# Kernel optimization log

Hardware: AMD Instinct MI355X
Metric: run time of the kernel (lower is better)

Reference implementation:

```python
import jax, jax.numpy as jnp
import numpy as np

B, T, N, D = 32, 50, 100, 4
E = N * (N - 1)
N_IN, N_HID, N_OUT = T * D, 256, 4


def _mlp(x, w1, b1, w2, b2):
    # Linear -> ReLU -> (dropout=0) -> Linear
    return jax.nn.relu(x @ w1 + b1) @ w2 + b2


def setup_inputs() -> dict:
    key = jax.random.key(0)
    ks = jax.random.split(key, 12)
    # fully-connected directed graph, no self loops
    idx = np.array([(i, j) for i in range(N) for j in range(N) if i != j], dtype=np.int64)
    recv, sendr = idx[:, 0], idx[:, 1]
    rec = jnp.asarray(np.eye(N, dtype=np.float32)[recv])    # [E, N]
    send = jnp.asarray(np.eye(N, dtype=np.float32)[sendr])  # [E, N]

    def lin(k, fan_in, fan_out):
        kw, kb = jax.random.split(k)
        w = jax.random.normal(kw, (fan_in, fan_out), jnp.float32) * 0.02
        b = jax.random.normal(kb, (fan_out,), jnp.float32) * 0.02
        return w, b

    x = jax.random.normal(ks[0], (B, T, N, D), jnp.float32)
    w1a, b1a = lin(ks[1], N_IN, N_HID)
    w1b, b1b = lin(ks[2], N_HID, N_HID)
    w2a, b2a = lin(ks[3], 2 * N_HID, N_HID)
    w2b, b2b = lin(ks[4], N_HID, N_HID)
    w3a, b3a = lin(ks[5], N_HID, N_HID)
    w3b, b3b = lin(ks[6], N_HID, N_HID)
    w4a, b4a = lin(ks[7], 3 * N_HID, N_HID)
    w4b, b4b = lin(ks[8], N_HID, N_HID)
    wo, bo = lin(ks[9], N_HID, N_OUT)
    return {"x": x, "rec": rec, "send": send,
            "w1a": w1a, "b1a": b1a, "w1b": w1b, "b1b": b1b,
            "w2a": w2a, "b2a": b2a, "w2b": w2b, "b2b": b2b,
            "w3a": w3a, "b3a": b3a, "w3b": w3b, "b3b": b3b,
            "w4a": w4a, "b4a": b4a, "w4b": w4b, "b4b": b4b,
            "wo": wo, "bo": bo}


def reference(x, rec, send,
              w1a, b1a, w1b, b1b,
              w2a, b2a, w2b, b2b,
              w3a, b3a, w3b, b3b,
              w4a, b4a, w4b, b4b,
              wo, bo):
    # [B, T, N, D] -> [B, N, T*D]
    h = jnp.transpose(x, (0, 2, 1, 3)).reshape(x.shape[0], x.shape[2], -1)
    h = _mlp(h, w1a, b1a, w1b, b1b)                       # [B, N, H]
    # v2e: gather receiver/sender node states to edges
    e = jnp.concatenate([jnp.einsum('en,bnh->beh', rec, h),
                         jnp.einsum('en,bnh->beh', send, h)], axis=2)  # [B, E, 2H]
    e = _mlp(e, w2a, b2a, w2b, b2b)                       # [B, E, H]
    x_skip = e
    # e2v: scatter edges back to nodes, normalize by n_nodes
    v = jnp.einsum('en,beh->bnh', rec, e) / e.shape[-2] * (e.shape[-2] / rec.shape[1])
    v = jnp.einsum('en,beh->bnh', rec, e) / rec.shape[1]  # incoming / incoming.size(1)=N
    v = _mlp(v, w3a, b3a, w3b, b3b)                       # [B, N, H]
    e2 = jnp.concatenate([jnp.einsum('en,bnh->beh', rec, v),
                          jnp.einsum('en,bnh->beh', send, v)], axis=2)  # [B, E, 2H]
    e2 = jnp.concatenate([e2, x_skip], axis=2)            # [B, E, 3H]
    e2 = _mlp(e2, w4a, b4a, w4b, b4b)                     # [B, E, H]
    return e2 @ wo + bo                                   # [B, E, n_out]
```

## Files before the change

kernel.cpp:

```cpp
#include <hip/hip_runtime.h>
#include <hip/hip_bf16.h>
#include <stdint.h>


typedef __attribute__((ext_vector_type(8))) short short8;
typedef __attribute__((ext_vector_type(4))) float float4v;
typedef __attribute__((ext_vector_type(4))) unsigned short ushort4v;

__device__ inline float bf2f(unsigned short u) {
    union { unsigned int i; float f; } v; v.i = ((unsigned int)u) << 16; return v.f;
}

#if __has_builtin(__builtin_amdgcn_cvt_pk_bf16_f32)
typedef __attribute__((ext_vector_type(2))) __bf16 bf16x2;
__device__ inline unsigned int f2bf_pk(float a, float b) {
    union { bf16x2 v; unsigned int u; } c;
    c.v = __builtin_amdgcn_cvt_pk_bf16_f32(a, b);
    return c.u;
}
__device__ inline unsigned short f2bf(float f) {
    return (unsigned short)(f2bf_pk(f, f) & 0xFFFFu);
}
#else
__device__ inline unsigned short f2bf(float f) {
    union { float f; unsigned int i; } v; v.f = f;
    unsigned int i = v.i;
    return (unsigned short)((i + 0x7FFFu + ((i >> 16) & 1u)) >> 16);
}
__device__ inline unsigned int f2bf_pk(float a, float b) {
    return (unsigned int)f2bf(a) | ((unsigned int)f2bf(b) << 16);
}
#endif

__global__ __launch_bounds__(256) void prep_kernel(
        const float* __restrict__ x,
        const float* __restrict__ w1a, const float* __restrict__ w1b,
        const float* __restrict__ w2a, const float* __restrict__ w2b,
        const float* __restrict__ w3a, const float* __restrict__ w3b,
        const float* __restrict__ w4a, const float* __restrict__ b4a,
        const float* __restrict__ w4b, const float* __restrict__ b4b,
        const float* __restrict__ wo,  const float* __restrict__ bo,
        const float* __restrict__ b2b,
        unsigned short* __restrict__ Wp1a, unsigned short* __restrict__ Wp1b,
        unsigned short* __restrict__ Wp2r, unsigned short* __restrict__ Wp2s,
        unsigned short* __restrict__ Wp2b, unsigned short* __restrict__ Wp3a,
        unsigned short* __restrict__ Wp3b, unsigned short* __restrict__ Wp4r,
        unsigned short* __restrict__ Wp4s, unsigned short* __restrict__ Wpz,
        unsigned short* __restrict__ Wfp, float* __restrict__ bfv,
        float* __restrict__ b4ap, float* __restrict__ b2bs,
        unsigned short* __restrict__ hin) {
    int bx = blockIdx.x;
    int tid = threadIdx.x;
    if (bx < 2272) {
        const float* W; unsigned short* Wp; int Kin; int b0;
        if      (bx <  224) { W = w1a;             Wp = Wp1a; Kin = 200; b0 = 0;    }
        else if (bx <  480) { W = w1b;             Wp = Wp1b; Kin = 256; b0 = 224;  }
        else if (bx <  736) { W = w2a;             Wp = Wp2r; Kin = 256; b0 = 480;  }
        else if (bx <  992) { W = w2a + 256 * 256; Wp = Wp2s; Kin = 256; b0 = 736;  }
        else if (bx < 1248) { W = w2b;             Wp = Wp2b; Kin = 256; b0 = 992;  }
        else if (bx < 1504) { W = w3a;             Wp = Wp3a; Kin = 256; b0 = 1248; }
        else if (bx < 1760) { W = w3b;             Wp = Wp3b; Kin = 256; b0 = 1504; }
        else if (bx < 2016) { W = w4a;             Wp = Wp4r; Kin = 256; b0 = 1760; }
        else                { W = w4a + 256 * 256; Wp = Wp4s; Kin = 256; b0 = 2016; }
        int idx = (bx - b0) * 256 + tid;
        int k = idx >> 8, n = idx & 255;
        unsigned short v = (k < Kin) ? f2bf(W[k * 256 + n]) : (unsigned short)0;
        Wp[((size_t)(k >> 5) * 256 + n) * 32 + (k & 31)] = v;
    } else if (bx < 2528) {
        int k = bx - 2272, c = tid;
        float s = 0.f;
        for (int t = 0; t < 256; ++t)
            s += w2b[k * 256 + t] * w4a[(size_t)(512 + t) * 256 + c];
        Wpz[((size_t)(k >> 5) * 256 + c) * 32 + (k & 31)] = f2bf(s);
    } else if (bx < 2530) {
        int k = tid;
        if (bx == 2528) {
            float a[4] = {0.f, 0.f, 0.f, 0.f};
            for (int c = 0; c < 256; ++c) {
                float wv = w4b[k * 256 + c];
                #pragma unroll
                for (int o = 0; o < 4; ++o) a[o] += wv * wo[c * 4 + o];
            }
            #pragma unroll
            for (int n = 0; n < 16; ++n)
                Wfp[(size_t)(k >> 5) * 512 + n * 32 + (k & 31)] =
                    (n < 4) ? f2bf(a[n]) : (unsigned short)0;
            if (k < 4) {
                float s = bo[k];
                for (int c = 0; c < 256; ++c) s += b4b[c] * wo[c * 4 + k];
                bfv[k] = s;
            }
        } else {
            float s = b4a[k];
            for (int t = 0; t < 256; ++t)
                s += b2b[t] * w4a[(size_t)(512 + t) * 256 + k];
            b4ap[k] = s;
            b2bs[k] = 0.99f * b2b[k];
        }
    } else {
        int idx = (bx - 2530) * 256 + tid;
        if (idx < 3200 * 224) {
            int row = idx / 224;
            int c = idx - row * 224;
            int b = row / 100, n = row - b * 100;
            unsigned short v = 0;
            if (c < 200) {
                int t = c >> 2, d = c & 3;
                v = f2bf(x[(((size_t)(b * 50 + t)) * 100 + n) * 4 + d]);
            }
            hin[(size_t)row * 224 + c] = v;
        }
    }
}

__global__ __launch_bounds__(512) void node_fusedA_kernel(
        const unsigned short* __restrict__ hin,
        const unsigned short* __restrict__ Wp1a, const float* __restrict__ b1a,
        const unsigned short* __restrict__ Wp1b, const float* __restrict__ b1b,
        const unsigned short* __restrict__ Wp2r, const float* __restrict__ b2a,
        const unsigned short* __restrict__ Wp2s,
        unsigned short* __restrict__ U, unsigned short* __restrict__ Hs) {
    __shared__ __align__(16) unsigned short t1s[16 * 264];
    __shared__ __align__(16) unsigned short hs2[16 * 264];
    const int m0 = blockIdx.x * 16;
    const int tid  = threadIdx.x;
    const int wave = tid >> 6;
    const int lane = tid & 63;
    const int l15  = lane & 15;
    const int quad = lane >> 4;
    const int n0   = wave * 32;
    const int koff = quad * 8;

    {
        float4v acc[2];
        acc[0] = (float4v)(0.0f); acc[1] = (float4v)(0.0f);
        for (int kb = 0; kb < 7; ++kb) {
            short8 af = *(const short8*)(hin + (size_t)(m0 + l15) * 224 + kb * 32 + koff);
            #pragma unroll
            for (int ni = 0; ni < 2; ++ni) {
                short8 bf = *(const short8*)(Wp1a + ((size_t)kb * 256 + n0 + ni * 16 + l15) * 32 + koff);
                acc[ni] = __builtin_amdgcn_mfma_f32_16x16x32_bf16(af, bf, acc[ni], 0, 0, 0);
            }
        }
        #pragma unroll
        for (int ni = 0; ni < 2; ++ni) {
            int col = n0 + ni * 16 + l15;
            float bv = b1a[col];
            #pragma unroll
            for (int r = 0; r < 4; ++r) {
                float v = acc[ni][r] + bv;
                v = v > 0.f ? v : 0.f;
                t1s[(quad * 4 + r) * 264 + col] = f2bf(v);
            }
        }
    }
    __syncthreads();

    {
        float4v acc[2];
        acc[0] = (float4v)(0.0f); acc[1] = (float4v)(0.0f);
        for (int kb = 0; kb < 8; ++kb) {
            short8 af = *(const short8*)(&t1s[l15 * 264 + kb * 32 + koff]);
            #pragma unroll
            for (int ni = 0; ni < 2; ++ni) {
                short8 bf = *(const short8*)(Wp1b + ((size_t)kb * 256 + n0 + ni * 16 + l15) * 32 + koff);
                acc[ni] = __builtin_amdgcn_mfma_f32_16x16x32_bf16(af, bf, acc[ni], 0, 0, 0);
            }
        }
        #pragma unroll
        for (int ni = 0; ni < 2; ++ni) {
            int col = n0 + ni * 16 + l15;
            float bv = b1b[col];
            #pragma unroll
            for (int r = 0; r < 4; ++r)
                hs2[(quad * 4 + r) * 264 + col] = f2bf(acc[ni][r] + bv);
        }
    }
    __syncthreads();

    {
        float4v aU[2], aH[2];
        aU[0] = (float4v)(0.0f); aU[1] = (float4v)(0.0f);
        aH[0] = (float4v)(0.0f); aH[1] = (float4v)(0.0f);
        for (int kb = 0; kb < 8; ++kb) {
            short8 af = *(const short8*)(&hs2[l15 * 264 + kb * 32 + koff]);
            #pragma unroll
            for (int ni = 0; ni < 2; ++ni) {
                short8 bu = *(const short8*)(Wp2r + ((size_t)kb * 256 + n0 + ni * 16 + l15) * 32 + koff);
                short8 bh = *(const short8*)(Wp2s + ((size_t)kb * 256 + n0 + ni * 16 + l15) * 32 + koff);
                aU[ni] = __builtin_amdgcn_mfma_f32_16x16x32_bf16(af, bu, aU[ni], 0, 0, 0);
                aH[ni] = __builtin_amdgcn_mfma_f32_16x16x32_bf16(af, bh, aH[ni], 0, 0, 0);
            }
        }
        #pragma unroll
        for (int ni = 0; ni < 2; ++ni) {
            int col = n0 + ni * 16 + l15;
            float bv = b2a[col];
            #pragma unroll
            for (int r = 0; r < 4; ++r) {
                size_t o = (size_t)(m0 + quad * 4 + r) * 256 + col;
                U[o]  = f2bf(aU[ni][r] + bv);
                Hs[o] = f2bf(aH[ni][r]);
            }
        }
    }
}

__global__ __launch_bounds__(512) void node_fusedC_kernel(
        const unsigned short* __restrict__ Ssc,
        const unsigned short* __restrict__ Wp2b, const float* __restrict__ b2bs,
        const unsigned short* __restrict__ Wp3a, const float* __restrict__ b3a,
        const unsigned short* __restrict__ Wp3b, const float* __restrict__ b3b,
        const unsigned short* __restrict__ Wp4r, const float* __restrict__ b4ap,
        const unsigned short* __restrict__ Wp4s,
        unsigned short* __restrict__ C4, unsigned short* __restrict__ Vs) {
    __shared__ __align__(16) unsigned short buf0[16 * 264];
    __shared__ __align__(16) unsigned short buf1[16 * 264];
    const int m0 = blockIdx.x * 16;
    const int tid  = threadIdx.x;
    const int wave = tid >> 6;
    const int lane = tid & 63;
    const int l15  = lane & 15;
    const int quad = lane >> 4;
    const int n0   = wave * 32;
    const int koff = quad * 8;

    {
        float4v acc[2];
        acc[0] = (float4v)(0.0f); acc[1] = (float4v)(0.0f);
        for (int kb = 0; kb < 8; ++kb) {
            short8 af = *(const short8*)(Ssc + (size_t)(m0 + l15) * 256 + kb * 32 + koff);
            #pragma unroll
            for (int ni = 0; ni < 2; ++ni) {
                short8 bf = *(const short8*)(Wp2b + ((size_t)kb * 256 + n0 + ni * 16 + l15) * 32 + koff);
                acc[ni] = __builtin_amdgcn_mfma_f32_16x16x32_bf16(af, bf, acc[ni], 0, 0, 0);
            }
        }
        #pragma unroll
        for (int ni = 0; ni < 2; ++ni) {
            int col = n0 + ni * 16 + l15;
            float bv = b2bs[col];
            #pragma unroll
            for (int r = 0; r < 4; ++r)
                buf0[(quad * 4 + r) * 264 + col] = f2bf(acc[ni][r] + bv);
        }
    }
    __syncthreads();

    {
        float4v acc[2];
        acc[0] = (float4v)(0.0f); acc[1] = (float4v)(0.0f);
        for (int kb = 0; kb < 8; ++kb) {
            short8 af = *(const short8*)(&buf0[l15 * 264 + kb * 32 + koff]);
            #pragma unroll
            for (int ni = 0; ni < 2; ++ni) {
                short8 bf = *(const short8*)(Wp3a + ((size_t)kb * 256 + n0 + ni * 16 + l15) * 32 + koff);
                acc[ni] = __builtin_amdgcn_mfma_f32_16x16x32_bf16(af, bf, acc[ni], 0, 0, 0);
            }
        }
        #pragma unroll
        for (int ni = 0; ni < 2; ++ni) {
            int col = n0 + ni * 16 + l15;
            float bv = b3a[col];
            #pragma unroll
            for (int r = 0; r < 4; ++r) {
                float v = acc[ni][r] + bv;
                v = v > 0.f ? v : 0.f;
                buf1[(quad * 4 + r) * 264 + col] = f2bf(v);
            }
        }
    }
    __syncthreads();

    {
        float4v acc[2];
        acc[0] = (float4v)(0.0f); acc[1] = (float4v)(0.0f);
        for (int kb = 0; kb < 8; ++kb) {
            short8 af = *(const short8*)(&buf1[l15 * 264 + kb * 32 + koff]);
            #pragma unroll
            for (int ni = 0; ni < 2; ++ni) {
                short8 bf = *(const short8*)(Wp3b + ((size_t)kb * 256 + n0 + ni * 16 + l15) * 32 + koff);
                acc[ni] = __builtin_amdgcn_mfma_f32_16x16x32_bf16(af, bf, acc[ni], 0, 0, 0);
            }
        }
        __syncthreads();
        #pragma unroll
        for (int ni = 0; ni < 2; ++ni) {
            int col = n0 + ni * 16 + l15;
            float bv = b3b[col];
            #pragma unroll
            for (int r = 0; r < 4; ++r)
                buf0[(quad * 4 + r) * 264 + col] = f2bf(acc[ni][r] + bv);
        }
    }
    __syncthreads();

    {
        float4v aC[2], aV[2];
        aC[0] = (float4v)(0.0f); aC[1] = (float4v)(0.0f);
        aV[0] = (float4v)(0.0f); aV[1] = (float4v)(0.0f);
        for (int kb = 0; kb < 8; ++kb) {
            short8 af = *(const short8*)(&buf0[l15 * 264 + kb * 32 + koff]);
            #pragma unroll
            for (int ni = 0; ni < 2; ++ni) {
                short8 bc = *(const short8*)(Wp4r + ((size_t)kb * 256 + n0 + ni * 16 + l15) * 32 + koff);
                short8 bv = *(const short8*)(Wp4s + ((size_t)kb * 256 + n0 + ni * 16 + l15) * 32 + koff);
                aC[ni] = __builtin_amdgcn_mfma_f32_16x16x32_bf16(af, bc, aC[ni], 0, 0, 0);
                aV[ni] = __builtin_amdgcn_mfma_f32_16x16x32_bf16(af, bv, aV[ni], 0, 0, 0);
            }
        }
        #pragma unroll
        for (int ni = 0; ni < 2; ++ni) {
            int col = n0 + ni * 16 + l15;
            float bv = b4ap[col];
            #pragma unroll
            for (int r = 0; r < 4; ++r) {
                size_t o = (size_t)(m0 + quad * 4 + r) * 256 + col;
                C4[o] = f2bf(aC[ni][r] + bv);
                Vs[o] = f2bf(aV[ni][r]);
            }
        }
    }
}

__global__ __launch_bounds__(256) void colsum_kernel(
        const unsigned short* __restrict__ U, const unsigned short* __restrict__ Hs,
        unsigned short* __restrict__ Ssc) {
    const int g = blockIdx.x * 4 + (threadIdx.x >> 6);
    const int b = g / 100, i = g - b * 100;
    const int c = (threadIdx.x & 63) * 4;
    ushort4v uv = *(const ushort4v*)(U + (size_t)g * 256 + c);
    const float u0 = bf2f(uv[0]), u1 = bf2f(uv[1]), u2 = bf2f(uv[2]), u3 = bf2f(uv[3]);
    const unsigned short* base = Hs + (size_t)b * 100 * 256 + c;
    float s0 = 0.f, s1 = 0.f, s2 = 0.f, s3 = 0.f;
    #pragma unroll 4
    for (int j = 0; j < 100; ++j) {
        ushort4v hv = *(const ushort4v*)(base + (size_t)j * 256);
        float v0 = u0 + bf2f(hv[0]); s0 += (v0 > 0.f ? v0 : 0.f);
        float v1 = u1 + bf2f(hv[1]); s1 += (v1 > 0.f ? v1 : 0.f);
        float v2 = u2 + bf2f(hv[2]); s2 += (v2 > 0.f ? v2 : 0.f);
        float v3 = u3 + bf2f(hv[3]); s3 += (v3 > 0.f ? v3 : 0.f);
    }
    {
        ushort4v hv = *(const ushort4v*)(base + (size_t)i * 256);
        float v0 = u0 + bf2f(hv[0]); s0 -= (v0 > 0.f ? v0 : 0.f);
        float v1 = u1 + bf2f(hv[1]); s1 -= (v1 > 0.f ? v1 : 0.f);
        float v2 = u2 + bf2f(hv[2]); s2 -= (v2 > 0.f ? v2 : 0.f);
        float v3 = u3 + bf2f(hv[3]); s3 -= (v3 > 0.f ? v3 : 0.f);
    }
    unsigned int* dst = (unsigned int*)(Ssc + (size_t)g * 256 + c);
    dst[0] = f2bf_pk(s0 * 0.01f, s1 * 0.01f);
    dst[1] = f2bf_pk(s2 * 0.01f, s3 * 0.01f);
}

__global__ __launch_bounds__(512, 6) void edge_phaseB_kernel(
        const unsigned short* __restrict__ Hs, const unsigned short* __restrict__ Vs,
        const unsigned short* __restrict__ U, const unsigned short* __restrict__ C4,
        const unsigned short* __restrict__ Wpz, const unsigned short* __restrict__ Wfp,
        const float* __restrict__ bfv,
        float* __restrict__ out) {
    __shared__ __align__(16) unsigned short t2s[64 * 264];
    const int g = blockIdx.x, hb = blockIdx.y;
    const int b = g / 100, nr = g - b * 100;
    const int nrows = hb ? 49 : 50;
    const int k0 = hb * 50;
    const int tid  = threadIdx.x;
    const int wave = tid >> 6;
    const int lane = tid & 63;
    const int l15  = lane & 15;
    const int quad = lane >> 4;
    const int n0   = wave * 32;
    const int koff = quad * 8;

    {
        const int c = lane * 4;
        ushort4v uv = *(const ushort4v*)(U + (size_t)g * 256 + c);
        float u0 = bf2f(uv[0]), u1 = bf2f(uv[1]), u2 = bf2f(uv[2]), u3 = bf2f(uv[3]);
        for (int r = wave; r < 64; r += 8) {
            unsigned int p01 = 0, p23 = 0;
            if (r < nrows) {
                int k = k0 + r;
                int j = k + (k >= nr ? 1 : 0);
                ushort4v hv = *(const ushort4v*)(Hs + (size_t)(b * 100 + j) * 256 + c);
                float t0 = u0 + bf2f(hv[0]); t0 = t0 > 0.f ? t0 : 0.f;
                float t1 = u1 + bf2f(hv[1]); t1 = t1 > 0.f ? t1 : 0.f;
                float t2 = u2 + bf2f(hv[2]); t2 = t2 > 0.f ? t2 : 0.f;
                float t3 = u3 + bf2f(hv[3]); t3 = t3 > 0.f ? t3 : 0.f;
                p01 = f2bf_pk(t0, t1);
                p23 = f2bf_pk(t2, t3);
            }
            unsigned int* dst = (unsigned int*)(&t2s[r * 264 + c]);
            dst[0] = p01;
            dst[1] = p23;
        }
    }
    __syncthreads();

    float4v acc[4][2];
    #pragma unroll
    for (int mi = 0; mi < 4; ++mi) {
        acc[mi][0] = (float4v)(0.0f);
        acc[mi][1] = (float4v)(0.0f);
    }

    #pragma unroll 1
    for (int kb = 0; kb < 8; ++kb) {
        short8 bf0 = *(const short8*)(Wpz + ((size_t)kb * 256 + n0 + l15) * 32 + koff);
        short8 bf1 = *(const short8*)(Wpz + ((size_t)kb * 256 + n0 + 16 + l15) * 32 + koff);
        #pragma unroll
        for (int mi = 0; mi < 4; ++mi) {
            short8 af = *(const short8*)(&t2s[(mi * 16 + l15) * 264 + kb * 32 + koff]);
            acc[mi][0] = __builtin_amdgcn_mfma_f32_16x16x32_bf16(af, bf0, acc[mi][0], 0, 0, 0);
            acc[mi][1] = __builtin_amdgcn_mfma_f32_16x16x32_bf16(af, bf1, acc[mi][1], 0, 0, 0);
        }
    }
    __syncthreads();

    {
        float c4v0 = bf2f(C4[(size_t)g * 256 + n0 + l15]);
        float c4v1 = bf2f(C4[(size_t)g * 256 + n0 + 16 + l15]);
        #pragma unroll
        for (int mi = 0; mi < 4; ++mi) {
            #pragma unroll
            for (int r = 0; r < 4; ++r) {
                int row = mi * 16 + quad * 4 + r;
                int k = k0 + row;
                int j = (row < nrows) ? (k + (k >= nr ? 1 : 0)) : 0;
                const unsigned short* vsr = Vs + (size_t)(b * 100 + j) * 256;
                float z0 = c4v0 + bf2f(vsr[n0 + l15]) + acc[mi][0][r];
                float z1 = c4v1 + bf2f(vsr[n0 + 16 + l15]) + acc[mi][1][r];
                z0 = z0 > 0.f ? z0 : 0.f;
                z1 = z1 > 0.f ? z1 : 0.f;
                unsigned int zp = f2bf_pk(z0, z1);
                t2s[row * 264 + n0 + l15]      = (unsigned short)zp;
                t2s[row * 264 + n0 + 16 + l15] = (unsigned short)(zp >> 16);
            }
        }
    }
    __syncthreads();

    if (wave < 4) {
        float4v pacc = (float4v)(0.0f);
        #pragma unroll
        for (int kb = 0; kb < 8; ++kb) {
            short8 za = *(const short8*)(&t2s[(wave * 16 + l15) * 264 + kb * 32 + koff]);
            short8 wb = *(const short8*)(Wfp + (size_t)kb * 512 + l15 * 32 + koff);
            pacc = __builtin_amdgcn_mfma_f32_16x16x32_bf16(za, wb, pacc, 0, 0, 0);
        }
        if (l15 < 4) {
            float bv = bfv[l15];
            #pragma unroll
            for (int r = 0; r < 4; ++r) {
                int row = wave * 16 + quad * 4 + r;
                if (row < nrows)
                    out[((size_t)b * 9900 + nr * 99 + k0 + row) * 4 + l15] = pacc[r] + bv;
            }
        }
    }
}

extern "C" void kernel_launch(void* const* d_in, const int* in_sizes, int n_in,
                              void* d_out, int out_size, void* d_ws, size_t ws_size,
                              hipStream_t stream) {
    const float* x   = (const float*)d_in[0];
    const float* w1a = (const float*)d_in[3];
    const float* b1a = (const float*)d_in[4];
    const float* w1b = (const float*)d_in[5];
    const float* b1b = (const float*)d_in[6];
    const float* w2a = (const float*)d_in[7];
    const float* b2a = (const float*)d_in[8];
    const float* w2b = (const float*)d_in[9];
    const float* b2b = (const float*)d_in[10];
    const float* w3a = (const float*)d_in[11];
    const float* b3a = (const float*)d_in[12];
    const float* w3b = (const float*)d_in[13];
    const float* b3b = (const float*)d_in[14];
    const float* w4a = (const float*)d_in[15];
    const float* b4a = (const float*)d_in[16];
    const float* w4b = (const float*)d_in[17];
    const float* b4b = (const float*)d_in[18];
    const float* wo  = (const float*)d_in[19];
    const float* bo  = (const float*)d_in[20];
    float* out = (float*)d_out;
    (void)in_sizes; (void)n_in; (void)out_size; (void)ws_size;

    char* ws = (char*)d_ws;
    size_t off = 0;
    auto alloc = [&](size_t bytes) {
        size_t o = off;
        off = (off + bytes + 255) & ~(size_t)255;
        return o;
    };
    const size_t SLOT_BF = (size_t)3200 * 256 * 2;
    unsigned short* S_U  = (unsigned short*)(ws + alloc(SLOT_BF));
    unsigned short* S_Hs = (unsigned short*)(ws + alloc(SLOT_BF));
    unsigned short* S_Vs = (unsigned short*)(ws + alloc(SLOT_BF));
    unsigned short* S_4  = (unsigned short*)(ws + alloc(SLOT_BF));
    unsigned short* Wp1a = (unsigned short*)(ws + alloc(224 * 256 * 2));
    unsigned short* Wp1b = (unsigned short*)(ws + alloc(256 * 256 * 2));
    unsigned short* Wp2r = (unsigned short*)(ws + alloc(256 * 256 * 2));
    unsigned short* Wp2s = (unsigned short*)(ws + alloc(256 * 256 * 2));
    unsigned short* Wp2b = (unsigned short*)(ws + alloc(256 * 256 * 2));
    unsigned short* Wp3a = (unsigned short*)(ws + alloc(256 * 256 * 2));
    unsigned short* Wp3b = (unsigned short*)(ws + alloc(256 * 256 * 2));
    unsigned short* Wp4r = (unsigned short*)(ws + alloc(256 * 256 * 2));
    unsigned short* Wp4s = (unsigned short*)(ws + alloc(256 * 256 * 2));
    unsigned short* Wpz  = (unsigned short*)(ws + alloc(256 * 256 * 2));
    unsigned short* Wfp  = (unsigned short*)(ws + alloc(8 * 16 * 32 * 2));
    float*          bfv  = (float*)(ws + alloc(4 * 4));
    float*          b4ap = (float*)(ws + alloc(256 * 4));
    float*          b2bs = (float*)(ws + alloc(256 * 4));

    unsigned short* hin = S_4;
    unsigned short* Ssc = S_4;
    unsigned short* C4  = S_4;

    hipLaunchKernelGGL(prep_kernel, dim3(5330), dim3(256), 0, stream,
                       x, w1a, w1b, w2a, w2b, w3a, w3b, w4a, b4a, w4b, b4b, wo, bo, b2b,
                       Wp1a, Wp1b, Wp2r, Wp2s, Wp2b, Wp3a, Wp3b, Wp4r, Wp4s, Wpz,
                       Wfp, bfv, b4ap, b2bs, hin);
    hipLaunchKernelGGL(node_fusedA_kernel, dim3(200), dim3(512), 0, stream,
                       hin, Wp1a, b1a, Wp1b, b1b, Wp2r, b2a, Wp2s, S_U, S_Hs);
    hipLaunchKernelGGL(colsum_kernel, dim3(800), dim3(256), 0, stream, S_U, S_Hs, Ssc);
    hipLaunchKernelGGL(node_fusedC_kernel, dim3(200), dim3(512), 0, stream,
                       Ssc, Wp2b, b2bs, Wp3a, b3a, Wp3b, b3b, Wp4r, b4ap, Wp4s, C4, S_Vs);
    hipLaunchKernelGGL(edge_phaseB_kernel, dim3(3200, 2), dim3(512), 0, stream,
                       S_Hs, S_Vs, S_U, C4, Wpz, Wfp, bfv, out);
}
```

Before: 256.2 us.

## Fuse edge-to-node column sum into node kernel and vectorize edge epilogue gathers

Folds the separate colsum kernel into node_fusedC, which now computes the scattered receiver sums into shared memory before its first GEMM. This removes one launch and the global round trip of Ssc. In the edge kernel, the Wpz columns are permuted so each lane handles adjacent column pairs, letting C4/Vs reads and t2s writes use 32-bit accesses. Gather row indices are also precomputed into a shared table. The fused node kernel runs only 200 blocks for the colsum work, so that work has less parallelism than before.

```diff
diff --git a/kernel.cpp b/kernel.cpp
--- a/kernel.cpp
+++ b/kernel.cpp
@@ -6,6 +6,7 @@
 typedef __attribute__((ext_vector_type(8))) short short8;
 typedef __attribute__((ext_vector_type(4))) float float4v;
 typedef __attribute__((ext_vector_type(4))) unsigned short ushort4v;
+typedef __attribute__((ext_vector_type(4))) unsigned int uint4v;
 
 __device__ inline float bf2f(unsigned short u) {
     union { unsigned int i; float f; } v; v.i = ((unsigned int)u) << 16; return v.f;
@@ -71,7 +72,8 @@
         float s = 0.f;
         for (int t = 0; t < 256; ++t)
             s += w2b[k * 256 + t] * w4a[(size_t)(512 + t) * 256 + c];
-        Wpz[((size_t)(k >> 5) * 256 + c) * 32 + (k & 31)] = f2bf(s);
+        int n = (c & ~31) + (c & 1) * 16 + ((c & 31) >> 1);
+        Wpz[((size_t)(k >> 5) * 256 + n) * 32 + (k & 31)] = f2bf(s);
     } else if (bx < 2530) {
         int k = tid;
         if (bx == 2528) {
@@ -207,7 +209,7 @@
 }
 
 __global__ __launch_bounds__(512) void node_fusedC_kernel(
-        const unsigned short* __restrict__ Ssc,
+        const unsigned short* __restrict__ U, const unsigned short* __restrict__ Hs,
         const unsigned short* __restrict__ Wp2b, const float* __restrict__ b2bs,
         const unsigned short* __restrict__ Wp3a, const float* __restrict__ b3a,
         const unsigned short* __restrict__ Wp3b, const float* __restrict__ b3b,
@@ -226,10 +228,53 @@
     const int koff = quad * 8;
 
     {
+        const int rl = tid >> 5;
+        const int ct = (tid & 31) * 8;
+        const int g = m0 + rl;
+        const int b = g / 100, i = g - b * 100;
+        float u[8], s[8];
+        {
+            ushort4v u0 = *(const ushort4v*)(U + (size_t)g * 256 + ct);
+            ushort4v u1 = *(const ushort4v*)(U + (size_t)g * 256 + ct + 4);
+            #pragma unroll
+            for (int e = 0; e < 4; ++e) { u[e] = bf2f(u0[e]); u[4 + e] = bf2f(u1[e]); }
+            #pragma unroll
+            for (int e = 0; e < 8; ++e) s[e] = 0.f;
+        }
+        const unsigned short* base = Hs + (size_t)b * 100 * 256 + ct;
+        #pragma unroll 4
+        for (int j = 0; j < 100; ++j) {
+            ushort4v h0 = *(const ushort4v*)(base + (size_t)j * 256);
+            ushort4v h1 = *(const ushort4v*)(base + (size_t)j * 256 + 4);
+            #pragma unroll
+            for (int e = 0; e < 4; ++e) {
+                float v0 = u[e] + bf2f(h0[e]);     s[e]     += (v0 > 0.f ? v0 : 0.f);
+                float v1 = u[4 + e] + bf2f(h1[e]); s[4 + e] += (v1 > 0.f ? v1 : 0.f);
+            }
+        }
+        {
+            ushort4v h0 = *(const ushort4v*)(base + (size_t)i * 256);
+            ushort4v h1 = *(const ushort4v*)(base + (size_t)i * 256 + 4);
+            #pragma unroll
+            for (int e = 0; e < 4; ++e) {
+                float v0 = u[e] + bf2f(h0[e]);     s[e]     -= (v0 > 0.f ? v0 : 0.f);
+                float v1 = u[4 + e] + bf2f(h1[e]); s[4 + e] -= (v1 > 0.f ? v1 : 0.f);
+            }
+        }
+        uint4v d;
+        d[0] = f2bf_pk(s[0] * 0.01f, s[1] * 0.01f);
+        d[1] = f2bf_pk(s[2] * 0.01f, s[3] * 0.01f);
+        d[2] = f2bf_pk(s[4] * 0.01f, s[5] * 0.01f);
+        d[3] = f2bf_pk(s[6] * 0.01f, s[7] * 0.01f);
+        *(uint4v*)(&buf1[rl * 264 + ct]) = d;
+    }
+    __syncthreads();
+
+    {
         float4v acc[2];
         acc[0] = (float4v)(0.0f); acc[1] = (float4v)(0.0f);
         for (int kb = 0; kb < 8; ++kb) {
-            short8 af = *(const short8*)(Ssc + (size_t)(m0 + l15) * 256 + kb * 32 + koff);
+            short8 af = *(const short8*)(&buf1[l15 * 264 + kb * 32 + koff]);
             #pragma unroll
             for (int ni = 0; ni < 2; ++ni) {
                 short8 bf = *(const short8*)(Wp2b + ((size_t)kb * 256 + n0 + ni * 16 + l15) * 32 + koff);
@@ -258,6 +303,7 @@
                 acc[ni] = __builtin_amdgcn_mfma_f32_16x16x32_bf16(af, bf, acc[ni], 0, 0, 0);
             }
         }
+        __syncthreads();
         #pragma unroll
         for (int ni = 0; ni < 2; ++ni) {
             int col = n0 + ni * 16 + l15;
@@ -321,36 +367,6 @@
             }
         }
     }
-}
-
-__global__ __launch_bounds__(256) void colsum_kernel(
-        const unsigned short* __restrict__ U, const unsigned short* __restrict__ Hs,
-        unsigned short* __restrict__ Ssc) {
-    const int g = blockIdx.x * 4 + (threadIdx.x >> 6);
-    const int b = g / 100, i = g - b * 100;
-    const int c = (threadIdx.x & 63) * 4;
-    ushort4v uv = *(const ushort4v*)(U + (size_t)g * 256 + c);
-    const float u0 = bf2f(uv[0]), u1 = bf2f(uv[1]), u2 = bf2f(uv[2]), u3 = bf2f(uv[3]);
-    const unsigned short* base = Hs + (size_t)b * 100 * 256 + c;
-    float s0 = 0.f, s1 = 0.f, s2 = 0.f, s3 = 0.f;
-    #pragma unroll 4
-    for (int j = 0; j < 100; ++j) {
-        ushort4v hv = *(const ushort4v*)(base + (size_t)j * 256);
-        float v0 = u0 + bf2f(hv[0]); s0 += (v0 > 0.f ? v0 : 0.f);
-        float v1 = u1 + bf2f(hv[1]); s1 += (v1 > 0.f ? v1 : 0.f);
-        float v2 = u2 + bf2f(hv[2]); s2 += (v2 > 0.f ? v2 : 0.f);
-        float v3 = u3 + bf2f(hv[3]); s3 += (v3 > 0.f ? v3 : 0.f);
-    }
-    {
-        ushort4v hv = *(const ushort4v*)(base + (size_t)i * 256);
-        float v0 = u0 + bf2f(hv[0]); s0 -= (v0 > 0.f ? v0 : 0.f);
-        float v1 = u1 + bf2f(hv[1]); s1 -= (v1 > 0.f ? v1 : 0.f);
-        float v2 = u2 + bf2f(hv[2]); s2 -= (v2 > 0.f ? v2 : 0.f);
-        float v3 = u3 + bf2f(hv[3]); s3 -= (v3 > 0.f ? v3 : 0.f);
-    }
-    unsigned int* dst = (unsigned int*)(Ssc + (size_t)g * 256 + c);
-    dst[0] = f2bf_pk(s0 * 0.01f, s1 * 0.01f);
-    dst[1] = f2bf_pk(s2 * 0.01f, s3 * 0.01f);
 }
 
 __global__ __launch_bounds__(512, 6) void edge_phaseB_kernel(
@@ -360,6 +376,7 @@
         const float* __restrict__ bfv,
         float* __restrict__ out) {
     __shared__ __align__(16) unsigned short t2s[64 * 264];
+    __shared__ int jtab[64];
     const int g = blockIdx.x, hb = blockIdx.y;
     const int b = g / 100, nr = g - b * 100;
     const int nrows = hb ? 49 : 50;
@@ -377,10 +394,11 @@
         ushort4v uv = *(const ushort4v*)(U + (size_t)g * 256 + c);
         float u0 = bf2f(uv[0]), u1 = bf2f(uv[1]), u2 = bf2f(uv[2]), u3 = bf2f(uv[3]);
         for (int r = wave; r < 64; r += 8) {
+            int k = k0 + r;
+            int j = (r < nrows) ? (k + (k >= nr ? 1 : 0)) : 0;
+            if (lane == 0) jtab[r] = b * 100 + j;
             unsigned int p01 = 0, p23 = 0;
             if (r < nrows) {
-                int k = k0 + r;
-                int j = k + (k >= nr ? 1 : 0);
                 ushort4v hv = *(const ushort4v*)(Hs + (size_t)(b * 100 + j) * 256 + c);
                 float t0 = u0 + bf2f(hv[0]); t0 = t0 > 0.f ? t0 : 0.f;
                 float t1 = u1 + bf2f(hv[1]); t1 = t1 > 0.f ? t1 : 0.f;
@@ -417,23 +435,22 @@
     __syncthreads();
 
     {
-        float c4v0 = bf2f(C4[(size_t)g * 256 + n0 + l15]);
-        float c4v1 = bf2f(C4[(size_t)g * 256 + n0 + 16 + l15]);
+        const int cp = n0 + 2 * l15;
+        unsigned int c4p = *(const unsigned int*)(C4 + (size_t)g * 256 + cp);
+        float c4v0 = bf2f((unsigned short)c4p);
+        float c4v1 = bf2f((unsigned short)(c4p >> 16));
         #pragma unroll
         for (int mi = 0; mi < 4; ++mi) {
             #pragma unroll
             for (int r = 0; r < 4; ++r) {
                 int row = mi * 16 + quad * 4 + r;
-                int k = k0 + row;
-                int j = (row < nrows) ? (k + (k >= nr ? 1 : 0)) : 0;
-                const unsigned short* vsr = Vs + (size_t)(b * 100 + j) * 256;
-                float z0 = c4v0 + bf2f(vsr[n0 + l15]) + acc[mi][0][r];
-                float z1 = c4v1 + bf2f(vsr[n0 + 16 + l15]) + acc[mi][1][r];
+                int jr = jtab[row];
+                unsigned int vsp = *(const unsigned int*)(Vs + (size_t)jr * 256 + cp);
+                float z0 = c4v0 + bf2f((unsigned short)vsp) + acc[mi][0][r];
+                float z1 = c4v1 + bf2f((unsigned short)(vsp >> 16)) + acc[mi][1][r];
                 z0 = z0 > 0.f ? z0 : 0.f;
                 z1 = z1 > 0.f ? z1 : 0.f;
-                unsigned int zp = f2bf_pk(z0, z1);
-                t2s[row * 264 + n0 + l15]      = (unsigned short)zp;
-                t2s[row * 264 + n0 + 16 + l15] = (unsigned short)(zp >> 16);
+                *(unsigned int*)(&t2s[row * 264 + cp]) = f2bf_pk(z0, z1);
             }
         }
     }
@@ -512,7 +529,6 @@
     float*          b2bs = (float*)(ws + alloc(256 * 4));
 
     unsigned short* hin = S_4;
-    unsigned short* Ssc = S_4;
     unsigned short* C4  = S_4;
 
     hipLaunchKernelGGL(prep_kernel, dim3(5330), dim3(256), 0, stream,
@@ -521,9 +537,8 @@
                        Wfp, bfv, b4ap, b2bs, hin);
     hipLaunchKernelGGL(node_fusedA_kernel, dim3(200), dim3(512), 0, stream,
                        hin, Wp1a, b1a, Wp1b, b1b, Wp2r, b2a, Wp2s, S_U, S_Hs);
-    hipLaunchKernelGGL(colsum_kernel, dim3(800), dim3(256), 0, stream, S_U, S_Hs, Ssc);
     hipLaunchKernelGGL(node_fusedC_kernel, dim3(200), dim3(512), 0, stream,
-                       Ssc, Wp2b, b2bs, Wp3a, b3a, Wp3b, b3b, Wp4r, b4ap, Wp4s, C4, S_Vs);
+                       S_U, S_Hs, Wp2b, b2bs, Wp3a, b3a, Wp3b, b3b, Wp4r, b4ap, Wp4s, C4, S_Vs);
     hipLaunchKernelGGL(edge_phaseB_kernel, dim3(3200, 2), dim3(512), 0, stream,
                        S_Hs, S_Vs, S_U, C4, Wpz, Wfp, bfv, out);
 }
```

Measured after the change: 249.1 us. 1.03x faster.
